# Kernel tuning notes

Hardware: AMD Instinct MI355X
Metric: run time of the kernel (lower is better)

## Reference

```python
import jax, jax.numpy as jnp
import numpy as np

N, DEG, NFEAT, NHID, NHEADS, NCLASS = 50000, 32, 512, 64, 8, 40
ALPHA = 0.2  # LeakyReLU negative slope


def _xavier(key, shape, gain=1.414):
    fan_in, fan_out = shape[-2], shape[-1]
    std = gain * np.sqrt(2.0 / (fan_in + fan_out))
    return (jax.random.normal(key, shape, dtype=jnp.float32) * std).astype(jnp.float32)


def setup_inputs() -> dict:
    key = jax.random.key(0)
    ks = jax.random.split(key, 9)
    E = N * DEG
    src = jax.random.randint(ks[0], (E,), 0, N, dtype=jnp.int32)
    dst = jax.random.randint(ks[1], (E,), 0, N, dtype=jnp.int32)
    loop = jnp.arange(N, dtype=jnp.int32)  # self-loops ensure nonzero rowsums
    edge = jnp.stack([jnp.concatenate([src, loop]), jnp.concatenate([dst, loop])])
    x = jax.random.normal(ks[2], (N, NFEAT), dtype=jnp.float32)
    return {
        "x": x,
        "edge": edge,  # [2, E+N] COO indices (row=target, col=source)
        "W": _xavier(ks[3], (NHEADS, NFEAT, NHID)),
        "W_pair": _xavier(ks[4], (NHEADS, 2 * NHID, NHID)),
        "a": _xavier(ks[5], (NHEADS, NHID, 1))[..., 0],  # [H, NHID]
        "W_out": _xavier(ks[6], (NHEADS * NHID, NCLASS)),
        "W_pair_out": _xavier(ks[7], (2 * NCLASS, NCLASS)),
        "a_out": _xavier(ks[8], (NCLASS, 1))[..., 0],  # [NCLASS]
    }


def _att_layer(x, src, dst, W, W_pair, a, concat):
    n = x.shape[0]
    d = W.shape[1]
    h = x @ W  # [N, d]
    # cat(h_src, h_dst) @ W_pair == h_src @ W_pair[:d] + h_dst @ W_pair[d:]
    z = jax.nn.leaky_relu(h[src] @ W_pair[:d] + h[dst] @ W_pair[d:], ALPHA)  # [E, d]
    e = jnp.exp(z @ a)  # [E]
    rowsum = jax.ops.segment_sum(e, src, num_segments=n)  # A @ ones
    h_prime = jax.ops.segment_sum(e[:, None] * h[dst], src, num_segments=n)  # A @ h
    h_prime = h_prime / rowsum[:, None]
    return jax.nn.elu(h_prime) if concat else h_prime


def reference(x, edge, W, W_pair, a, W_out, W_pair_out, a_out):
    src, dst = edge[0], edge[1]
    heads = [_att_layer(x, src, dst, W[i], W_pair[i], a[i], True) for i in range(NHEADS)]
    x2 = jax.nn.elu(jnp.concatenate(heads, axis=1))  # [N, H*NHID]
    out = jax.nn.elu(_att_layer(x2, src, dst, W_out, W_pair_out, a_out, False))
    return out  # [N, NCLASS]
```

## Files before the change

### kernel.cpp

```cpp
#include <hip/hip_runtime.h>
#include <hip/hip_bf16.h>
#include <hip/hip_fp16.h>

typedef _Float16 f16;
typedef _Float16 f16x2 __attribute__((ext_vector_type(2)));
typedef _Float16 f16x8 __attribute__((ext_vector_type(8)));
typedef float f32x4 __attribute__((ext_vector_type(4)));

#define HEADS 8
#define HID 64
#define NCLS 40
#define FEAT 512

__global__ void pack_all(const float* __restrict__ W, const float* __restrict__ Wp,
                         const float* __restrict__ Wo, const float* __restrict__ Wpo,
                         f16* __restrict__ Wh_t, f16* __restrict__ Bp_t,
                         f16* __restrict__ Wo_t, float* __restrict__ B2p) {
    int idx = blockIdx.x * blockDim.x + threadIdx.x;
    if (idx < 512 * 512) {
        int c = idx >> 9, k = idx & 511;
        Wh_t[idx] = (f16)W[(c >> 6) * 512 * 64 + k * 64 + (c & 63)];
    } else if (idx < 512 * 512 + 8 * 128 * 64) {
        int i = idx - 512 * 512;
        int head = i >> 13, c = (i >> 6) & 127, k = i & 63;
        Bp_t[i] = (f16)Wp[head * 8192 + ((c >> 6) * 64 + k) * 64 + (c & 63)];
    } else if (idx < 512 * 512 + 8 * 128 * 64 + 40 * 512) {
        int i = idx - (512 * 512 + 8 * 128 * 64);
        int c = i >> 9, k = i & 511;
        Wo_t[i] = (f16)Wo[k * 40 + c];
    } else if (idx < 512 * 512 + 8 * 128 * 64 + 40 * 512 + 40 * 80) {
        int i = idx - (512 * 512 + 8 * 128 * 64 + 40 * 512);
        int k = i / 80, c = i % 80;
        int p = c / 40, j = c % 40;
        B2p[i] = Wpo[(p * 40 + k) * 40 + j];
    }
}

__global__ void pack_vh2(const float* __restrict__ h2, const float* __restrict__ uv2,
                         f16x2* __restrict__ vh2, int total) {
    int i = blockIdx.x * blockDim.x + threadIdx.x;
    if (i >= total) return;
    int t = i / 40, k = i % 40;
    vh2[i] = f16x2{(f16)uv2[(size_t)t * 80 + 40 + k], (f16)h2[i]};
}

__global__ void hist_kernel(const int* __restrict__ src, int* __restrict__ counts, int ne) {
    int i = blockIdx.x * blockDim.x + threadIdx.x;
    int stride = gridDim.x * blockDim.x;
    for (; i < ne; i += stride) atomicAdd(&counts[src[i]], 1);
}

__global__ void scan_partial(const int* __restrict__ counts, int* __restrict__ partial, int n) {
    __shared__ int s[256];
    int i = blockIdx.x * 256 + threadIdx.x;
    s[threadIdx.x] = (i < n) ? counts[i] : 0;
    __syncthreads();
    for (int d = 128; d > 0; d >>= 1) {
        if (threadIdx.x < d) s[threadIdx.x] += s[threadIdx.x + d];
        __syncthreads();
    }
    if (threadIdx.x == 0) partial[blockIdx.x] = s[0];
}

__global__ void scan_top(int* __restrict__ partial, int nb) {
    __shared__ int s[1024];
    int tid = threadIdx.x;
    s[tid] = (tid < nb) ? partial[tid] : 0;
    __syncthreads();
    for (int d = 1; d < 1024; d <<= 1) {
        int v = (tid >= d) ? s[tid - d] : 0;
        __syncthreads();
        s[tid] += v;
        __syncthreads();
    }
    if (tid < nb) partial[tid] = (tid == 0) ? 0 : s[tid - 1];
}

__global__ void scan_final(const int* __restrict__ counts, const int* __restrict__ partialEx,
                           int* __restrict__ offsets, int* __restrict__ cursor, int n) {
    __shared__ int s[256];
    int i = blockIdx.x * 256 + threadIdx.x;
    int v = (i < n) ? counts[i] : 0;
    s[threadIdx.x] = v;
    __syncthreads();
    for (int d = 1; d < 256; d <<= 1) {
        int u = (threadIdx.x >= d) ? s[threadIdx.x - d] : 0;
        __syncthreads();
        s[threadIdx.x] += u;
        __syncthreads();
    }
    int excl = partialEx[blockIdx.x] + s[threadIdx.x] - v;
    if (i < n) {
        cursor[i] = excl;
        offsets[i] = excl;
        if (i == n - 1) offsets[n] = excl + v;
    }
}

__global__ void scatter_kernel(const int* __restrict__ src, const int* __restrict__ dst,
                               int* __restrict__ cursor, int* __restrict__ dsts, int ne) {
    int i = blockIdx.x * blockDim.x + threadIdx.x;
    int stride = gridDim.x * blockDim.x;
    for (; i < ne; i += stride) {
        int pos = atomicAdd(&cursor[src[i]], 1);
        dsts[pos] = dst[i];
    }
}

__device__ __forceinline__ void stC(float* p, float v) { *p = v; }
__device__ __forceinline__ void stC(f16* p, float v) { *p = (f16)v; }
__device__ __forceinline__ f16x8 ldA8(const f16* p) { return *(const f16x8*)p; }
__device__ __forceinline__ f16x8 ldA8(const float* p) {
    float4 a = ((const float4*)p)[0];
    float4 b = ((const float4*)p)[1];
    f16x8 r = {(f16)a.x, (f16)a.y, (f16)a.z, (f16)a.w, (f16)b.x, (f16)b.y, (f16)b.z, (f16)b.w};
    return r;
}

template <typename AT, typename CT>
__global__ __launch_bounds__(256)
void gemm_mfma(const AT* __restrict__ A, int lda, int acol0, int acolStride,
               const f16* __restrict__ Bt, long bBatchStride, int K,
               CT* __restrict__ C, int ldc, int ccolStride,
               int nrows, int ncols) {
    __shared__ f16 As[128][40];
    __shared__ f16 Bs[128][40];
    const int batch = blockIdx.y;
    const int row0 = blockIdx.x * 128;
    const int col0 = blockIdx.z * 128;
    const int a0 = acol0 + batch * acolStride;
    const f16* Bb = Bt + (size_t)batch * bBatchStride;
    const int tid = threadIdx.x;
    const int lane = tid & 63;
    const int wave = tid >> 6;
    const int wr = (wave >> 1) * 64;
    const int wc = (wave & 1) * 64;
    f32x4 acc[4][4] = {};

    for (int k0 = 0; k0 < K; k0 += 32) {
#pragma unroll
        for (int i = 0; i < 2; i++) {
            int idx = tid + i * 256;
            int r = idx >> 2, ch = idx & 3;
            int gr = row0 + r;
            f16x8 val = {};
            if (gr < nrows) val = ldA8(A + (size_t)gr * lda + a0 + k0 + ch * 8);
            *(f16x8*)(&As[r][ch * 8]) = val;
        }
#pragma unroll
        for (int i = 0; i < 2; i++) {
            int idx = tid + i * 256;
            int r = idx >> 2, ch = idx & 3;
            int gc = col0 + r;
            f16x8 val = {};
            if (gc < ncols) val = *(const f16x8*)(Bb + (size_t)gc * K + k0 + ch * 8);
            *(f16x8*)(&Bs[r][ch * 8]) = val;
        }
        __syncthreads();
        f16x8 af[4], bf[4];
#pragma unroll
        for (int t = 0; t < 4; t++)
            af[t] = *(const f16x8*)(&As[wr + t * 16 + (lane & 15)][(lane >> 4) * 8]);
#pragma unroll
        for (int t = 0; t < 4; t++)
            bf[t] = *(const f16x8*)(&Bs[wc + t * 16 + (lane & 15)][(lane >> 4) * 8]);
#pragma unroll
        for (int i = 0; i < 4; i++)
#pragma unroll
            for (int j = 0; j < 4; j++)
                acc[i][j] = __builtin_amdgcn_mfma_f32_16x16x32_f16(af[i], bf[j], acc[i][j], 0, 0, 0);
        __syncthreads();
    }
    const int crow = (lane >> 4) * 4;
    const int ccol = lane & 15;
#pragma unroll
    for (int i = 0; i < 4; i++) {
#pragma unroll
        for (int j = 0; j < 4; j++) {
            int gc = col0 + wc + j * 16 + ccol;
            if (gc >= ncols) continue;
#pragma unroll
            for (int r = 0; r < 4; r++) {
                int gr = row0 + wr + i * 16 + crow + r;
                if (gr < nrows)
                    stC(&C[(size_t)gr * ldc + (size_t)batch * ccolStride + gc], acc[i][j][r]);
            }
        }
    }
}

__global__ void gemm_kernel(const float* __restrict__ A, int lda,
                            const float* __restrict__ B, int ldb,
                            float* __restrict__ C, int ldc,
                            int nrows, int K, int ncols) {
    __shared__ __align__(16) float As[16][68];
    __shared__ __align__(16) float Bs[16][64];
    const int colblk = blockIdx.z * 64;
    const int row0 = blockIdx.x * 64;
    const int tid = threadIdx.x;
    const int tm = tid >> 4, tn = tid & 15;
    float acc[4][4] = {};
    for (int k0 = 0; k0 < K; k0 += 16) {
#pragma unroll
        for (int i = 0; i < 4; i++) {
            int idx = tid + i * 256;
            int m = idx >> 4;
            int k = idx & 15;
            int gr = row0 + m;
            float v = 0.f;
            if (gr < nrows && (k0 + k) < K) v = A[(size_t)gr * lda + k0 + k];
            As[k][m] = v;
        }
#pragma unroll
        for (int i = 0; i < 4; i++) {
            int idx = tid + i * 256;
            int k = idx >> 6;
            int j = idx & 63;
            float v = 0.f;
            if ((k0 + k) < K && (colblk + j) < ncols) v = B[(size_t)(k0 + k) * ldb + colblk + j];
            Bs[k][j] = v;
        }
        __syncthreads();
#pragma unroll
        for (int k = 0; k < 16; k++) {
            float av[4], bv[4];
#pragma unroll
            for (int i = 0; i < 4; i++) av[i] = As[k][tm * 4 + i];
#pragma unroll
            for (int j = 0; j < 4; j++) bv[j] = Bs[k][tn * 4 + j];
#pragma unroll
            for (int i = 0; i < 4; i++)
#pragma unroll
                for (int j = 0; j < 4; j++) acc[i][j] += av[i] * bv[j];
        }
        __syncthreads();
    }
#pragma unroll
    for (int i = 0; i < 4; i++) {
        int gr = row0 + tm * 4 + i;
        if (gr >= nrows) continue;
#pragma unroll
        for (int j = 0; j < 4; j++) {
            int gc = colblk + tn * 4 + j;
            if (gc < ncols) C[(size_t)gr * ldc + gc] = acc[i][j];
        }
    }
}

__device__ __forceinline__ void store8h(f16* p, const float o[8]) {
    f16x8 v;
#pragma unroll
    for (int k = 0; k < 8; k++) v[k] = (f16)o[k];
    *(f16x8*)p = v;
}

__device__ __forceinline__ float dot8_lrelu(const uint4& vr, const f16x2 u2[4],
                                            const f16x2 a2[4]) {
    const f16x2* vp = (const f16x2*)&vr;
    float p = 0.f;
#pragma unroll
    for (int k = 0; k < 4; k++) {
        f16x2 w = u2[k] + vp[k];
        f16x2 lr = __builtin_elementwise_max(w, w * (_Float16)0.2f);
#if __has_builtin(__builtin_amdgcn_fdot2)
        p = __builtin_amdgcn_fdot2(lr, a2[k], p, false);
#else
        p = fmaf((float)lr[0], (float)a2[k][0], p);
        p = fmaf((float)lr[1], (float)a2[k][1], p);
#endif
    }
    return p;
}

__global__ void edge_l1(const int* __restrict__ offsets, const int* __restrict__ dsts,
                        const f16* __restrict__ h, const f16* __restrict__ uv,
                        const float* __restrict__ a, f16* __restrict__ x2, int n) {
    const int lane = threadIdx.x & 63;
    const int wave = threadIdx.x >> 6;
    const int t = blockIdx.x * (blockDim.x >> 6) + wave;
    if (t >= n) return;
    const int head = lane >> 3;
    const int sub = lane & 7;
    const unsigned voff = head * 128 + 64 + sub * 8;
    const unsigned uoff = head * 128 + sub * 8;
    const unsigned hoff = lane * 8;

    f16x2 u2[4], a2[4];
    {
        uint4 ur = *(const uint4*)(uv + (size_t)t * 1024 + uoff);
        const f16x2* up = (const f16x2*)&ur;
#pragma unroll
        for (int k = 0; k < 4; k++) u2[k] = up[k];
        const float4* ap = (const float4*)(a + hoff);
        float4 a0 = ap[0], a1 = ap[1];
        a2[0] = f16x2{(f16)a0.x, (f16)a0.y};
        a2[1] = f16x2{(f16)a0.z, (f16)a0.w};
        a2[2] = f16x2{(f16)a1.x, (f16)a1.y};
        a2[3] = f16x2{(f16)a1.z, (f16)a1.w};
    }

    const int s0 = offsets[t], s1 = offsets[t + 1];
    float acc[8] = {0.f, 0.f, 0.f, 0.f, 0.f, 0.f, 0.f, 0.f};
    float rs = 0.f;

    for (int base = s0; base < s1; base += 64) {
        int cnt = s1 - base;
        if (cnt > 64) cnt = 64;
        int myd = (lane < cnt) ? dsts[base + lane] : 0;
        int d0 = __shfl(myd, 0, 64);
        uint4 vr = *(const uint4*)(uv + (size_t)(unsigned)d0 * 1024 + voff);
        uint4 hr = *(const uint4*)(h + (size_t)(unsigned)d0 * 512 + hoff);
        for (int j = 0; j < cnt; j++) {
            uint4 vr_n, hr_n;
            if (j + 1 < cnt) {
                int dn = __shfl(myd, j + 1, 64);
                vr_n = *(const uint4*)(uv + (size_t)(unsigned)dn * 1024 + voff);
                hr_n = *(const uint4*)(h + (size_t)(unsigned)dn * 512 + hoff);
            }
            float p = dot8_lrelu(vr, u2, a2);
            p += __shfl_xor(p, 1, 64);
            p += __shfl_xor(p, 2, 64);
            p += __shfl_xor(p, 4, 64);
            float wgt = __expf(p);
            rs += wgt;
            const f16* hp = (const f16*)&hr;
#pragma unroll
            for (int k = 0; k < 8; k++) acc[k] = fmaf(wgt, (float)hp[k], acc[k]);
            vr = vr_n;
            hr = hr_n;
        }
    }
    float inv = 1.f / rs;
    float o[8];
#pragma unroll
    for (int k = 0; k < 8; k++) {
        float hp = acc[k] * inv;
        float e1 = hp > 0.f ? hp : expm1f(hp);
        o[k] = e1 > 0.f ? e1 : expm1f(e1);
    }
    store8h(x2 + (size_t)t * 512 + hoff, o);
}

__global__ void edge_l2(const int* __restrict__ offsets, const int* __restrict__ dsts,
                        const f16x2* __restrict__ vh2, const float* __restrict__ uv2,
                        const float* __restrict__ a_out, float* __restrict__ out, int n) {
    const int lane = threadIdx.x & 63;
    const int wave = threadIdx.x >> 6;
    const int t = blockIdx.x * (blockDim.x >> 6) + wave;
    if (t >= n) return;
    const int g = lane >> 3;
    const int s = lane & 7;
    float u5[5], a5[5];
#pragma unroll
    for (int k = 0; k < 5; k++) {
        u5[k] = uv2[(size_t)t * 80 + s * 5 + k];
        a5[k] = a_out[s * 5 + k];
    }
    const int s0 = offsets[t], s1 = offsets[t + 1];
    float acc[5] = {0.f, 0.f, 0.f, 0.f, 0.f};
    float rs = 0.f;
    for (int base = s0; base < s1; base += 64) {
        int cnt = s1 - base;
        if (cnt > 64) cnt = 64;
        int myd = (lane < cnt) ? dsts[base + lane] : 0;
        for (int j8 = 0; j8 < cnt; j8 += 8) {
            int eidx = j8 + g;
            bool active = eidx < cnt;
            int d = __shfl(myd, active ? eidx : 0, 64);
            f16x2 vh[5];
            const f16x2* vp = vh2 + (size_t)(unsigned)d * 40 + s * 5;
#pragma unroll
            for (int k = 0; k < 5; k++) vh[k] = vp[k];
            float p = 0.f;
#pragma unroll
            for (int k = 0; k < 5; k++) {
                float w = u5[k] + (float)vh[k][0];
                p = fmaf(a5[k], fmaxf(w, 0.2f * w), p);
            }
            p += __shfl_xor(p, 1, 64);
            p += __shfl_xor(p, 2, 64);
            p += __shfl_xor(p, 4, 64);
            float wgt = active ? __expf(p) : 0.f;
            rs += wgt;
#pragma unroll
            for (int k = 0; k < 5; k++) acc[k] = fmaf(wgt, (float)vh[k][1], acc[k]);
        }
    }
    rs += __shfl_xor(rs, 8, 64);
    rs += __shfl_xor(rs, 16, 64);
    rs += __shfl_xor(rs, 32, 64);
#pragma unroll
    for (int k = 0; k < 5; k++) {
        acc[k] += __shfl_xor(acc[k], 8, 64);
        acc[k] += __shfl_xor(acc[k], 16, 64);
        acc[k] += __shfl_xor(acc[k], 32, 64);
    }
    if (g == 0) {
        float inv = 1.f / rs;
#pragma unroll
        for (int k = 0; k < 5; k++) {
            float hp = acc[k] * inv;
            out[(size_t)t * 40 + s * 5 + k] = hp > 0.f ? hp : expm1f(hp);
        }
    }
}

extern "C" void kernel_launch(void* const* d_in, const int* in_sizes, int n_in,
                              void* d_out, int out_size, void* d_ws, size_t ws_size,
                              hipStream_t stream) {
    const float* x         = (const float*)d_in[0];
    const int*   edge      = (const int*)d_in[1];
    const float* W         = (const float*)d_in[2];
    const float* W_pair    = (const float*)d_in[3];
    const float* a         = (const float*)d_in[4];
    const float* W_out     = (const float*)d_in[5];
    const float* W_pair_out= (const float*)d_in[6];
    const float* a_out     = (const float*)d_in[7];
    float* out = (float*)d_out;

    const int n  = in_sizes[0] / FEAT;
    const int ne = in_sizes[1] / 2;
    const int* srcArr = edge;
    const int* dstArr = edge + ne;

    char* ws = (char*)d_ws;
    size_t off = 0;
    auto alloc = [&](size_t bytes) -> void* {
        void* p = ws + off;
        off = (off + bytes + 255) & ~(size_t)255;
        return p;
    };
    f16* h    = (f16*)alloc((size_t)n * 512 * sizeof(f16));
    f16* uv   = (f16*)alloc((size_t)n * 1024 * sizeof(f16));
    f16* x2   = (f16*)alloc((size_t)n * 512 * sizeof(f16));
    f16x2* vh2 = (f16x2*)alloc((size_t)n * 40 * sizeof(f16x2));
    f16* Wh_t = (f16*)alloc(512 * 512 * sizeof(f16));
    f16* Bp_t = (f16*)alloc(8 * 128 * 64 * sizeof(f16));
    f16* Wo_t = (f16*)alloc(40 * 512 * sizeof(f16));
    float* B2p = (float*)alloc(40 * 80 * sizeof(float));
    int* counts  = (int*)alloc((size_t)n * sizeof(int));
    int* offsets = (int*)alloc((size_t)(n + 1) * sizeof(int));
    int* cursor  = (int*)alloc((size_t)n * sizeof(int));
    int* partial = (int*)alloc(1024 * sizeof(int));
    int* dsts    = (int*)alloc((size_t)ne * sizeof(int));
    float* h2  = (float*)h;
    float* uv2 = (float*)((char*)h + (size_t)n * 40 * sizeof(float));

    const int nb = (n + 255) / 256;

    hipMemsetAsync(counts, 0, (size_t)n * sizeof(int), stream);
    hist_kernel<<<2048, 256, 0, stream>>>(srcArr, counts, ne);
    scan_partial<<<nb, 256, 0, stream>>>(counts, partial, n);
    scan_top<<<1, 1024, 0, stream>>>(partial, nb);
    scan_final<<<nb, 256, 0, stream>>>(counts, partial, offsets, cursor, n);
    scatter_kernel<<<2048, 256, 0, stream>>>(srcArr, dstArr, cursor, dsts, ne);

    const int packTotal = 512 * 512 + 8 * 128 * 64 + 40 * 512 + 40 * 80;
    pack_all<<<(packTotal + 255) / 256, 256, 0, stream>>>(
        W, W_pair, W_out, W_pair_out, Wh_t, Bp_t, Wo_t, B2p);

    const int mBlocks = (n + 127) / 128;

    gemm_mfma<float, f16><<<dim3(mBlocks, 1, 4), 256, 0, stream>>>(
        x, 512, 0, 0, Wh_t, 0, 512, h, 512, 0, n, 512);

    gemm_mfma<f16, f16><<<dim3(mBlocks, 8, 1), 256, 0, stream>>>(
        h, 512, 0, 64, Bp_t, 128L * 64, 64, uv, 1024, 128, n, 128);

    edge_l1<<<dim3((n + 3) / 4), 256, 0, stream>>>(offsets, dsts, h, uv, a, x2, n);

    gemm_mfma<f16, float><<<dim3(mBlocks, 1, 1), 256, 0, stream>>>(
        x2, 512, 0, 0, Wo_t, 0, 512, h2, 40, 0, n, 40);

    gemm_kernel<<<dim3((n + 63) / 64, 1, 2), 256, 0, stream>>>(
        h2, 40, B2p, 80, uv2, 80, n, 40, 80);

    pack_vh2<<<(n * 40 + 255) / 256, 256, 0, stream>>>(h2, uv2, vh2, n * 40);

    edge_l2<<<dim3((n + 3) / 4), 256, 0, stream>>>(offsets, dsts, vh2, uv2, a_out, out, n);
}
```

Before: 925.9 us.

## Split layer-1 edge kernel into attention-weight and aggregation passes

Splits the fused layer-1 edge kernel into two kernels. The first computes per-edge, per-head exp attention weights from the uv gather and writes them to a new global buffer. The second gathers h rows and accumulates the weighted sums with the softmax normalisation. The likely aim is less register pressure and fewer concurrent gathers per kernel, so each pass gets more memory-level parallelism. The cost is an extra launch, a second walk over the CSR indices, and writing then reading an E×8 float weight array (about 52 MB).

```diff
diff --git a/kernel.cpp b/kernel.cpp
--- a/kernel.cpp
+++ b/kernel.cpp
@@ -272,9 +272,9 @@
     return p;
 }
 
-__global__ void edge_l1(const int* __restrict__ offsets, const int* __restrict__ dsts,
-                        const f16* __restrict__ h, const f16* __restrict__ uv,
-                        const float* __restrict__ a, f16* __restrict__ x2, int n) {
+__global__ void edge_w(const int* __restrict__ offsets, const int* __restrict__ dsts,
+                       const f16* __restrict__ uv, const float* __restrict__ a,
+                       float* __restrict__ wgtArr, int n) {
     const int lane = threadIdx.x & 63;
     const int wave = threadIdx.x >> 6;
     const int t = blockIdx.x * (blockDim.x >> 6) + wave;
@@ -283,7 +283,6 @@
     const int sub = lane & 7;
     const unsigned voff = head * 128 + 64 + sub * 8;
     const unsigned uoff = head * 128 + sub * 8;
-    const unsigned hoff = lane * 8;
 
     f16x2 u2[4], a2[4];
     {
@@ -291,7 +290,7 @@
         const f16x2* up = (const f16x2*)&ur;
 #pragma unroll
         for (int k = 0; k < 4; k++) u2[k] = up[k];
-        const float4* ap = (const float4*)(a + hoff);
+        const float4* ap = (const float4*)(a + head * 64 + sub * 8);
         float4 a0 = ap[0], a1 = ap[1];
         a2[0] = f16x2{(f16)a0.x, (f16)a0.y};
         a2[1] = f16x2{(f16)a0.z, (f16)a0.w};
@@ -300,34 +299,63 @@
     }
 
     const int s0 = offsets[t], s1 = offsets[t + 1];
-    float acc[8] = {0.f, 0.f, 0.f, 0.f, 0.f, 0.f, 0.f, 0.f};
-    float rs = 0.f;
-
     for (int base = s0; base < s1; base += 64) {
         int cnt = s1 - base;
         if (cnt > 64) cnt = 64;
         int myd = (lane < cnt) ? dsts[base + lane] : 0;
         int d0 = __shfl(myd, 0, 64);
         uint4 vr = *(const uint4*)(uv + (size_t)(unsigned)d0 * 1024 + voff);
-        uint4 hr = *(const uint4*)(h + (size_t)(unsigned)d0 * 512 + hoff);
         for (int j = 0; j < cnt; j++) {
-            uint4 vr_n, hr_n;
+            uint4 vr_n;
             if (j + 1 < cnt) {
                 int dn = __shfl(myd, j + 1, 64);
                 vr_n = *(const uint4*)(uv + (size_t)(unsigned)dn * 1024 + voff);
-                hr_n = *(const uint4*)(h + (size_t)(unsigned)dn * 512 + hoff);
             }
             float p = dot8_lrelu(vr, u2, a2);
             p += __shfl_xor(p, 1, 64);
             p += __shfl_xor(p, 2, 64);
             p += __shfl_xor(p, 4, 64);
-            float wgt = __expf(p);
-            rs += wgt;
+            if (sub == 0) wgtArr[(size_t)(base + j) * 8 + head] = __expf(p);
+            vr = vr_n;
+        }
+    }
+}
+
+__global__ void edge_agg(const int* __restrict__ offsets, const int* __restrict__ dsts,
+                         const f16* __restrict__ h, const float* __restrict__ wgtArr,
+                         f16* __restrict__ x2, int n) {
+    const int lane = threadIdx.x & 63;
+    const int wave = threadIdx.x >> 6;
+    const int t = blockIdx.x * (blockDim.x >> 6) + wave;
+    if (t >= n) return;
+    const int head = lane >> 3;
+    const unsigned hoff = lane * 8;
+
+    const int s0 = offsets[t], s1 = offsets[t + 1];
+    float acc[8] = {0.f, 0.f, 0.f, 0.f, 0.f, 0.f, 0.f, 0.f};
+    float rs = 0.f;
+
+    for (int base = s0; base < s1; base += 64) {
+        int cnt = s1 - base;
+        if (cnt > 64) cnt = 64;
+        int myd = (lane < cnt) ? dsts[base + lane] : 0;
+        int d0 = __shfl(myd, 0, 64);
+        uint4 hr = *(const uint4*)(h + (size_t)(unsigned)d0 * 512 + hoff);
+        float w0 = wgtArr[(size_t)base * 8 + head];
+        for (int j = 0; j < cnt; j++) {
+            uint4 hr_n;
+            float w_n;
+            if (j + 1 < cnt) {
+                int dn = __shfl(myd, j + 1, 64);
+                hr_n = *(const uint4*)(h + (size_t)(unsigned)dn * 512 + hoff);
+                w_n = wgtArr[(size_t)(base + j + 1) * 8 + head];
+            }
+            rs += w0;
             const f16* hp = (const f16*)&hr;
 #pragma unroll
-            for (int k = 0; k < 8; k++) acc[k] = fmaf(wgt, (float)hp[k], acc[k]);
-            vr = vr_n;
+            for (int k = 0; k < 8; k++) acc[k] = fmaf(w0, (float)hp[k], acc[k]);
             hr = hr_n;
+            w0 = w_n;
         }
     }
     float inv = 1.f / rs;
@@ -433,6 +461,7 @@
     f16* h    = (f16*)alloc((size_t)n * 512 * sizeof(f16));
     f16* uv   = (f16*)alloc((size_t)n * 1024 * sizeof(f16));
     f16* x2   = (f16*)alloc((size_t)n * 512 * sizeof(f16));
+    float* wgt = (float*)alloc((size_t)ne * 8 * sizeof(float));
     f16x2* vh2 = (f16x2*)alloc((size_t)n * 40 * sizeof(f16x2));
     f16* Wh_t = (f16*)alloc(512 * 512 * sizeof(f16));
     f16* Bp_t = (f16*)alloc(8 * 128 * 64 * sizeof(f16));
@@ -467,7 +496,8 @@
     gemm_mfma<f16, f16><<<dim3(mBlocks, 8, 1), 256, 0, stream>>>(
         h, 512, 0, 64, Bp_t, 128L * 64, 64, uv, 1024, 128, n, 128);
 
-    edge_l1<<<dim3((n + 3) / 4), 256, 0, stream>>>(offsets, dsts, h, uv, a, x2, n);
+    edge_w<<<dim3((n + 3) / 4), 256, 0, stream>>>(offsets, dsts, uv, a, wgt, n);
+    edge_agg<<<dim3((n + 3) / 4), 256, 0, stream>>>(offsets, dsts, h, wgt, x2, n);
 
     gemm_mfma<f16, float><<<dim3(mBlocks, 1, 1), 256, 0, stream>>>(
         x2, 512, 0, 0, Wo_t, 0, 512, h2, 40, 0, n, 40);
```

After: 944.9 us. 1.02x slower.

## Replace per-row atomic CSR scatter with two-level bucket scatter plus LDS placement

Applied to the files above, without the earlier changes.

The single scatter pass, which did one global atomic per edge on a per-row cursor with random writes, becomes two passes. The first pass groups edges into 256-row buckets using a small array of bucket cursors and writes (src,dst) pairs. The second pass places each bucket's edges in shared memory with LDS atomics and then writes them out coalesced. This removes scattered global atomics and random stores, at the cost of an extra pairs buffer, an extra kernel pass, and heavy atomic contention on only ~196 bucket counters.

```diff
diff --git a/kernel.cpp b/kernel.cpp
--- a/kernel.cpp
+++ b/kernel.cpp
@@ -11,6 +11,8 @@
 #define HID 64
 #define NCLS 40
 #define FEAT 512
+#define BKT 256
+#define WINCAP 12288
 
 __global__ void pack_all(const float* __restrict__ W, const float* __restrict__ Wp,
                          const float* __restrict__ Wo, const float* __restrict__ Wpo,
@@ -77,7 +79,7 @@
 }
 
 __global__ void scan_final(const int* __restrict__ counts, const int* __restrict__ partialEx,
-                           int* __restrict__ offsets, int* __restrict__ cursor, int n) {
+                           int* __restrict__ offsets, int n) {
     __shared__ int s[256];
     int i = blockIdx.x * 256 + threadIdx.x;
     int v = (i < n) ? counts[i] : 0;
@@ -91,19 +93,53 @@
     }
     int excl = partialEx[blockIdx.x] + s[threadIdx.x] - v;
     if (i < n) {
-        cursor[i] = excl;
         offsets[i] = excl;
         if (i == n - 1) offsets[n] = excl + v;
     }
 }
 
-__global__ void scatter_kernel(const int* __restrict__ src, const int* __restrict__ dst,
-                               int* __restrict__ cursor, int* __restrict__ dsts, int ne) {
+__global__ void binit(const int* __restrict__ offsets, int* __restrict__ bcursor, int nbuckets) {
+    int b = blockIdx.x * blockDim.x + threadIdx.x;
+    if (b < nbuckets) bcursor[b] = offsets[b * BKT];
+}
+
+__global__ void bucket_scatter(const int* __restrict__ src, const int* __restrict__ dst,
+                               int* __restrict__ bcursor, uint2* __restrict__ pairs, int ne) {
     int i = blockIdx.x * blockDim.x + threadIdx.x;
     int stride = gridDim.x * blockDim.x;
     for (; i < ne; i += stride) {
-        int pos = atomicAdd(&cursor[src[i]], 1);
-        dsts[pos] = dst[i];
+        int s = src[i];
+        int pos = atomicAdd(&bcursor[s >> 8], 1);
+        pairs[pos] = uint2{(unsigned)s, (unsigned)dst[i]};
+    }
+}
+
+__global__ void lds_place(const uint2* __restrict__ pairs, const int* __restrict__ offsets,
+                          int* __restrict__ dsts, int n) {
+    __shared__ int cnt[BKT];
+    __shared__ int win[WINCAP];
+    const int b = blockIdx.x;
+    const int t0 = b * BKT;
+    const int t1 = (t0 + BKT < n) ? t0 + BKT : n;
+    const int base = offsets[t0];
+    const int end = offsets[t1];
+    const int m = end - base;
+    for (int t = threadIdx.x; t < t1 - t0; t += blockDim.x) cnt[t] = offsets[t0 + t] - base;
+    __syncthreads();
+    if (m <= WINCAP) {
+        for (int i = threadIdx.x; i < m; i += blockDim.x) {
+            uint2 p = pairs[base + i];
+            int pos = atomicAdd(&cnt[p.x - (unsigned)t0], 1);
+            win[pos] = (int)p.y;
+        }
+        __syncthreads();
+        for (int i = threadIdx.x; i < m; i += blockDim.x) dsts[base + i] = win[i];
+    } else {
+        for (int i = threadIdx.x; i < m; i += blockDim.x) {
+            uint2 p = pairs[base + i];
+            int pos = atomicAdd(&cnt[p.x - (unsigned)t0], 1);
+            dsts[base + pos] = (int)p.y;
+        }
     }
 }
 
@@ -434,26 +470,30 @@
     f16* uv   = (f16*)alloc((size_t)n * 1024 * sizeof(f16));
     f16* x2   = (f16*)alloc((size_t)n * 512 * sizeof(f16));
     f16x2* vh2 = (f16x2*)alloc((size_t)n * 40 * sizeof(f16x2));
+    uint2* pairs = (uint2*)alloc((size_t)ne * sizeof(uint2));
     f16* Wh_t = (f16*)alloc(512 * 512 * sizeof(f16));
     f16* Bp_t = (f16*)alloc(8 * 128 * 64 * sizeof(f16));
     f16* Wo_t = (f16*)alloc(40 * 512 * sizeof(f16));
     float* B2p = (float*)alloc(40 * 80 * sizeof(float));
     int* counts  = (int*)alloc((size_t)n * sizeof(int));
     int* offsets = (int*)alloc((size_t)(n + 1) * sizeof(int));
-    int* cursor  = (int*)alloc((size_t)n * sizeof(int));
+    int* bcursor = (int*)alloc(1024 * sizeof(int));
     int* partial = (int*)alloc(1024 * sizeof(int));
     int* dsts    = (int*)alloc((size_t)ne * sizeof(int));
     float* h2  = (float*)h;
     float* uv2 = (float*)((char*)h + (size_t)n * 40 * sizeof(float));
 
     const int nb = (n + 255) / 256;
+    const int nbuckets = (n + BKT - 1) / BKT;
 
     hipMemsetAsync(counts, 0, (size_t)n * sizeof(int), stream);
     hist_kernel<<<2048, 256, 0, stream>>>(srcArr, counts, ne);
     scan_partial<<<nb, 256, 0, stream>>>(counts, partial, n);
     scan_top<<<1, 1024, 0, stream>>>(partial, nb);
-    scan_final<<<nb, 256, 0, stream>>>(counts, partial, offsets, cursor, n);
-    scatter_kernel<<<2048, 256, 0, stream>>>(srcArr, dstArr, cursor, dsts, ne);
+    scan_final<<<nb, 256, 0, stream>>>(counts, partial, offsets, n);
+    binit<<<(nbuckets + 255) / 256, 256, 0, stream>>>(offsets, bcursor, nbuckets);
+    bucket_scatter<<<2048, 256, 0, stream>>>(srcArr, dstArr, bcursor, pairs, ne);
+    lds_place<<<nbuckets, 256, 0, stream>>>(pairs, offsets, dsts, n);
 
     const int packTotal = 512 * 512 + 8 * 128 * 64 + 40 * 512 + 40 * 80;
     pack_all<<<(packTotal + 255) / 256, 256, 0, stream>>>(
```

Result: slower. 1.790 ms (+93.3%).
